# Kernel tuning notes

Measured on AMD Instinct MI355X. Metric: run time of the kernel, lower is better.

The kernel has to match this reference:

```python
import jax, jax.numpy as jnp
import numpy as np

EPS = 1e-12  # torch F.normalize eps
K = 32       # num_clusters (hardcoded in module)

def l2norm(v, axis):
    n = jnp.sqrt(jnp.sum(v * v, axis=axis, keepdims=True))
    return v / jnp.maximum(n, EPS)

def setup_inputs() -> dict:
    key = jax.random.key(0)
    k1, k2, k3, k4 = jax.random.split(key, 4)
    B, M, D = 64, 128, 2048
    x = jax.random.normal(k1, (B, M, D), dtype=jnp.float32)
    # ragged lengths in [1, M]
    lengths = jax.random.randint(k2, (B,), 0, M, dtype=jnp.int32) + 1
    init_sc = 1.0 / np.sqrt(D)
    W = init_sc * jax.random.normal(k3, (K, D), dtype=jnp.float32)  # fc1.weight
    C = init_sc * jax.random.normal(k4, (K, D), dtype=jnp.float32)  # centroids
    return {"x": x, "lengths": lengths, "W": W, "C": C}

def reference(x, lengths, W, C):
    # x: [B,M,D] padded frames, lengths: [B] valid frame counts
    B, M, D = x.shape
    mask = (jnp.arange(M)[None, :] < lengths[:, None]).astype(x.dtype)  # [B,M]
    cnt = lengths.astype(x.dtype)[:, None]                              # [B,1]
    # avg pooling over valid (raw, un-normalized) frames
    avgpool = jnp.sum(x * mask[:, :, None], axis=1) / cnt               # [B,D]
    # per-frame L2 normalize
    xn = l2norm(x, axis=-1)                                             # [B,M,D]
    # soft assignment: linear (no bias) + softmax over clusters
    logits = jnp.einsum('bmd,kd->bmk', xn, W)
    a = jax.nn.softmax(logits, axis=-1) * mask[:, :, None]              # [B,M,K]
    # VLAD residual aggregation, GEMM form:
    # sum_m a[b,m,k]*(xn[b,m,:] - C[k,:]) = (a^T xn) - C * sum_m a
    ax = jnp.einsum('bmk,bmd->bkd', a, xn)                              # [B,K,D]
    asum = jnp.sum(a, axis=1)                                           # [B,K]
    vlad = ax - asum[:, :, None] * C[None, :, :]                        # [B,K,D]
    # intra-normalize per cluster, flatten, global L2 normalize
    vlad = l2norm(vlad, axis=2)
    vlad = vlad.reshape(B, K * D)
    vlad = l2norm(vlad, axis=1)
    return jnp.concatenate([avgpool, vlad], axis=1)                     # [B, D + K*D]
```

## Files before the change

kernel.cpp:

```cpp
#include <hip/hip_runtime.h>
#include <math.h>

#define BB 64
#define MM 128
#define DDIM 2048
#define KK 32
#define NFR (BB*MM)
#define OUTROW (DDIM + KK*DDIM)

typedef __attribute__((ext_vector_type(8))) short bf16x8;
typedef __attribute__((ext_vector_type(4))) float f32x4;

__device__ __forceinline__ short f2bf(float f) {
  unsigned u = __builtin_bit_cast(unsigned, f);
  u += 0x7fffu + ((u >> 16) & 1u);
  return (short)(u >> 16);
}
__device__ __forceinline__ unsigned pack2(float lo, float hi) {
  return (unsigned)(unsigned short)f2bf(lo) | ((unsigned)(unsigned short)f2bf(hi) << 16);
}

__global__ __launch_bounds__(256) void k_prep(const float* __restrict__ W,
                                              short* __restrict__ Wb) {
  int i = (blockIdx.x * 256 + threadIdx.x) * 8;
  float4 a = *(const float4*)(W + i);
  float4 b = *(const float4*)(W + i + 4);
  bf16x8 o = {f2bf(a.x), f2bf(a.y), f2bf(a.z), f2bf(a.w),
              f2bf(b.x), f2bf(b.y), f2bf(b.z), f2bf(b.w)};
  *(bf16x8*)(Wb + i) = o;
}

__global__ __launch_bounds__(256, 2) void k_logits(const float* __restrict__ x,
    const int* __restrict__ lengths, const short* __restrict__ Wb,
    short* __restrict__ aT, float* __restrict__ asum_p) {
  const int t = threadIdx.x, wv = t >> 6, lane = t & 63;
  const int l15 = lane & 15, quad = lane >> 4;
  const int fg = blockIdx.x;
  const int g0 = fg * 16;
  const int b  = fg >> 3;
  const int m0 = (fg & 7) * 16;
  const int len = lengths[b];
  const bool av = (m0 + l15) < len;

  const float* xrow = x + (size_t)(g0 + l15) * DDIM + wv * 512 + quad * 8;
  const short* w0   = Wb + l15 * DDIM + wv * 512 + quad * 8;
  const short* w1   = w0 + 16 * DDIM;

  f32x4 c0 = {0.f, 0.f, 0.f, 0.f}, c1 = {0.f, 0.f, 0.f, 0.f};
  float ssq = 0.f;
  #pragma unroll
  for (int h = 0; h < 2; ++h) {
    float4 xa[8], xc[8];
    bf16x8 B0[8], B1[8];
    #pragma unroll
    for (int s = 0; s < 8; ++s) {
      const int so = h * 8 + s;
      if (av) {
        xa[s] = *(const float4*)(xrow + so * 32);
        xc[s] = *(const float4*)(xrow + so * 32 + 4);
      } else {
        xa[s] = make_float4(0.f, 0.f, 0.f, 0.f);
        xc[s] = make_float4(0.f, 0.f, 0.f, 0.f);
      }
      B0[s] = *(const bf16x8*)(w0 + so * 32);
      B1[s] = *(const bf16x8*)(w1 + so * 32);
    }
    #pragma unroll
    for (int s = 0; s < 8; ++s) {
      ssq = fmaf(xa[s].x, xa[s].x, ssq); ssq = fmaf(xa[s].y, xa[s].y, ssq);
      ssq = fmaf(xa[s].z, xa[s].z, ssq); ssq = fmaf(xa[s].w, xa[s].w, ssq);
      ssq = fmaf(xc[s].x, xc[s].x, ssq); ssq = fmaf(xc[s].y, xc[s].y, ssq);
      ssq = fmaf(xc[s].z, xc[s].z, ssq); ssq = fmaf(xc[s].w, xc[s].w, ssq);
      bf16x8 A = {f2bf(xa[s].x), f2bf(xa[s].y), f2bf(xa[s].z), f2bf(xa[s].w),
                  f2bf(xc[s].x), f2bf(xc[s].y), f2bf(xc[s].z), f2bf(xc[s].w)};
      c0 = __builtin_amdgcn_mfma_f32_16x16x32_bf16(A, B0[s], c0, 0, 0, 0);
      c1 = __builtin_amdgcn_mfma_f32_16x16x32_bf16(A, B1[s], c1, 0, 0, 0);
    }
  }

  ssq += __shfl_xor(ssq, 16, 64);
  ssq += __shfl_xor(ssq, 32, 64);
  __shared__ float sq[4][16];
  __shared__ float lg[4][16][33];
  if (quad == 0) sq[wv][l15] = ssq;
  #pragma unroll
  for (int r = 0; r < 4; ++r) {
    lg[wv][quad * 4 + r][l15]      = c0[r];
    lg[wv][quad * 4 + r][16 + l15] = c1[r];
  }
  __syncthreads();

  const int fr = t >> 4, kk = (t & 15) * 2;
  float s0 = 0.f, s1 = 0.f;
  #pragma unroll
  for (int w = 0; w < 4; ++w) { s0 += lg[w][fr][kk]; s1 += lg[w][fr][kk + 1]; }
  float ss  = sq[0][fr] + sq[1][fr] + sq[2][fr] + sq[3][fr];
  float inv = 1.f / fmaxf(sqrtf(ss), 1e-12f);
  s0 *= inv; s1 *= inv;
  float mx = fmaxf(s0, s1);
  mx = fmaxf(mx, __shfl_xor(mx, 1, 64));
  mx = fmaxf(mx, __shfl_xor(mx, 2, 64));
  mx = fmaxf(mx, __shfl_xor(mx, 4, 64));
  mx = fmaxf(mx, __shfl_xor(mx, 8, 64));
  float e0 = __expf(s0 - mx), e1 = __expf(s1 - mx);
  float se = e0 + e1;
  se += __shfl_xor(se, 1, 64);
  se += __shfl_xor(se, 2, 64);
  se += __shfl_xor(se, 4, 64);
  se += __shfl_xor(se, 8, 64);
  const bool valid = (m0 + fr) < len;
  float rr = valid ? (1.f / se) : 0.f;
  float a0 = e0 * rr, a1 = e1 * rr;

  __syncthreads();
  lg[0][fr][kk] = a0; lg[0][fr][kk + 1] = a1;
  __syncthreads();
  if (t < KK) {
    float s = 0.f;
    #pragma unroll
    for (int f = 0; f < 16; ++f) s += lg[0][f][t];
    asum_p[(size_t)fg * KK + t] = s;
  }
  short* ap = aT + (size_t)b * KK * MM + m0 + fr;
  ap[(size_t)kk * MM]       = f2bf(a0 * inv);
  ap[(size_t)(kk + 1) * MM] = f2bf(a1 * inv);
}

__global__ __launch_bounds__(256, 2) void k_vlad(const float* __restrict__ x,
    const int* __restrict__ lengths, const float* __restrict__ Cc,
    const short* __restrict__ aT, const float* __restrict__ asum_p,
    float* __restrict__ out, float* __restrict__ ssq_part) {
  const int t = threadIdx.x, wv = t >> 6, lane = t & 63;
  const int l15 = lane & 15, quad = lane >> 4;
  const int dc = blockIdx.x, b = blockIdx.y;
  const int dw0 = dc * 256 + wv * 64;
  const int len = lengths[b];

  __shared__ short xbt[4][64][40];
  __shared__ float asl[KK];
  __shared__ float ssw[4][33];

  if (t < KK) {
    float s = 0.f;
    #pragma unroll
    for (int p = 0; p < 8; ++p) s += asum_p[(size_t)(b * 8 + p) * KK + t];
    asl[t] = s;
  }

  const float* xb  = x  + (size_t)b * MM * DDIM;
  const short* at0 = aT + (size_t)b * KK * MM + l15 * MM + quad * 8;

  const int q4   = l15 * 4;
  const int mrow = quad * 2;
  const int keyw = l15 & 3;
  const int keyr = (l15 >> 2) & 3;

  bf16x8 A0[4], A1[4];
  #pragma unroll
  for (int ms = 0; ms < 4; ++ms) {
    A0[ms] = *(const bf16x8*)(at0 + ms * 32);
    A1[ms] = *(const bf16x8*)(at0 + 16 * MM + ms * 32);
  }

  float4 v0[16], v1[16];
  #pragma unroll
  for (int ms = 0; ms < 4; ++ms) {
    #pragma unroll
    for (int p = 0; p < 4; ++p) {
      const int m = ms * 32 + p * 8 + mrow;
      const float* xr = xb + (size_t)m * DDIM + dw0 + q4;
      v0[ms * 4 + p] = (m < len) ? *(const float4*)xr
                                 : make_float4(0.f, 0.f, 0.f, 0.f);
      v1[ms * 4 + p] = (m + 1 < len) ? *(const float4*)(xr + DDIM)
                                     : make_float4(0.f, 0.f, 0.f, 0.f);
    }
  }

  float avg[4] = {0.f, 0.f, 0.f, 0.f};
  #pragma unroll
  for (int i = 0; i < 16; ++i) {
    avg[0] += v0[i].x + v1[i].x;
    avg[1] += v0[i].y + v1[i].y;
    avg[2] += v0[i].z + v1[i].z;
    avg[3] += v0[i].w + v1[i].w;
  }

  f32x4 acc[2][4];
  #pragma unroll
  for (int kt = 0; kt < 2; ++kt)
    #pragma unroll
    for (int nt = 0; nt < 4; ++nt) acc[kt][nt] = (f32x4){0.f, 0.f, 0.f, 0.f};

  #pragma unroll
  for (int ms = 0; ms < 4; ++ms) {
    #pragma unroll
    for (int p = 0; p < 4; ++p) {
      const int i = ms * 4 + p;
      const int mls = (p ^ keyw) * 8 + mrow;
      *(unsigned*)&xbt[wv][q4 + 0][mls] = pack2(v0[i].x, v1[i].x);
      *(unsigned*)&xbt[wv][q4 + 1][mls] = pack2(v0[i].y, v1[i].y);
      *(unsigned*)&xbt[wv][q4 + 2][mls] = pack2(v0[i].z, v1[i].z);
      *(unsigned*)&xbt[wv][q4 + 3][mls] = pack2(v0[i].w, v1[i].w);
    }
    #pragma unroll
    for (int nt = 0; nt < 4; ++nt) {
      bf16x8 B = *(const bf16x8*)&xbt[wv][nt * 16 + l15][(quad ^ keyr) * 8];
      acc[0][nt] = __builtin_amdgcn_mfma_f32_16x16x32_bf16(A0[ms], B, acc[0][nt], 0, 0, 0);
      acc[1][nt] = __builtin_amdgcn_mfma_f32_16x16x32_bf16(A1[ms], B, acc[1][nt], 0, 0, 0);
    }
  }

  #pragma unroll
  for (int c = 0; c < 4; ++c) {
    avg[c] += __shfl_xor(avg[c], 16, 64);
    avg[c] += __shfl_xor(avg[c], 32, 64);
  }
  if (quad == 0) {
    float rl = 1.f / (float)len;
    *(float4*)(out + (size_t)b * OUTROW + dw0 + q4) =
        make_float4(avg[0] * rl, avg[1] * rl, avg[2] * rl, avg[3] * rl);
  }

  __syncthreads();
  float* orow = out + (size_t)b * OUTROW + DDIM;
  #pragma unroll
  for (int kt = 0; kt < 2; ++kt) {
    #pragma unroll
    for (int r = 0; r < 4; ++r) {
      const int k = kt * 16 + quad * 4 + r;
      const float as = asl[k];
      float sqv = 0.f;
      #pragma unroll
      for (int nt = 0; nt < 4; ++nt) {
        const int d = dw0 + nt * 16 + l15;
        float v = acc[kt][nt][r] - as * Cc[(size_t)k * DDIM + d];
        orow[(size_t)k * DDIM + d] = v;
        sqv = fmaf(v, v, sqv);
      }
      sqv += __shfl_xor(sqv, 1, 64);
      sqv += __shfl_xor(sqv, 2, 64);
      sqv += __shfl_xor(sqv, 4, 64);
      sqv += __shfl_xor(sqv, 8, 64);
      if (l15 == 0) ssw[wv][k] = sqv;
    }
  }
  __syncthreads();
  if (t < KK)
    ssq_part[((size_t)dc * BB + b) * KK + t] =
        ssw[0][t] + ssw[1][t] + ssw[2][t] + ssw[3][t];
}

__global__ __launch_bounds__(256) void k_norm(const float* __restrict__ ssq_part,
    float* __restrict__ out) {
  const int t = threadIdx.x;
  const int k = blockIdx.x;
  const int b = blockIdx.y;
  __shared__ float ssk[32];
  if (t < 32) {
    float sk = 0.f;
    #pragma unroll
    for (int dc = 0; dc < 8; ++dc)
      sk += ssq_part[((size_t)dc * BB + b) * KK + t];
    ssk[t] = sk;
  }
  __syncthreads();
  float gss = 0.f, iv_own = 0.f;
  #pragma unroll
  for (int kk = 0; kk < 32; ++kk) {
    float nk = sqrtf(ssk[kk]);
    float iv = 1.f / fmaxf(nk, 1e-12f);
    float nn = nk * iv;
    gss += nn * nn;
    if (kk == k) iv_own = iv;
  }
  float sc = iv_own / fmaxf(sqrtf(gss), 1e-12f);
  float* row = out + (size_t)b * OUTROW + DDIM + (size_t)k * DDIM;
  #pragma unroll
  for (int h = 0; h < 2; ++h) {
    float4* p = (float4*)(row + h * 1024 + t * 4);
    float4 v = *p;
    v.x *= sc; v.y *= sc; v.z *= sc; v.w *= sc;
    *p = v;
  }
}

extern "C" void kernel_launch(void* const* d_in, const int* in_sizes, int n_in,
                              void* d_out, int out_size, void* d_ws, size_t ws_size,
                              hipStream_t stream) {
  const float* x       = (const float*)d_in[0];
  const int*   lengths = (const int*)d_in[1];
  const float* W       = (const float*)d_in[2];
  const float* C       = (const float*)d_in[3];
  float* out = (float*)d_out;

  short* Wb     = (short*)d_ws;
  short* aT     = Wb + (size_t)KK * DDIM;
  float* asum_p = (float*)(aT + (size_t)BB * KK * MM);
  float* ssqp   = asum_p + (size_t)512 * KK;

  k_prep  <<<dim3(32),     256, 0, stream>>>(W, Wb);
  k_logits<<<dim3(512),    256, 0, stream>>>(x, lengths, Wb, aT, asum_p);
  k_vlad  <<<dim3(8, BB),  256, 0, stream>>>(x, lengths, C, aT, asum_p, out, ssqp);
  k_norm  <<<dim3(KK, BB), 256, 0, stream>>>(ssqp, out);
}
```

Before: 145.5 us.

## Fuse logits, VLAD, and normalization into one kernel with per-batch spin barriers

Measured after the change: 402.9 us. 2.77x slower.

```diff
diff --git a/kernel.cpp b/kernel.cpp
--- a/kernel.cpp
+++ b/kernel.cpp
@@ -5,7 +5,6 @@
 #define MM 128
 #define DDIM 2048
 #define KK 32
-#define NFR (BB*MM)
 #define OUTROW (DDIM + KK*DDIM)
 
 typedef __attribute__((ext_vector_type(8))) short bf16x8;
@@ -18,6 +17,21 @@
 }
 __device__ __forceinline__ unsigned pack2(float lo, float hi) {
   return (unsigned)(unsigned short)f2bf(lo) | ((unsigned)(unsigned short)f2bf(hi) << 16);
+}
+
+__device__ __forceinline__ void batch_barrier(int* bar) {
+  __syncthreads();
+  __threadfence();
+  if (threadIdx.x == 0) {
+    __hip_atomic_fetch_add(bar, 1, __ATOMIC_ACQ_REL, __HIP_MEMORY_SCOPE_AGENT);
+    int it = 0;
+    while (__hip_atomic_load(bar, __ATOMIC_ACQUIRE, __HIP_MEMORY_SCOPE_AGENT) < 8) {
+      __builtin_amdgcn_s_sleep(8);
+      if (++it > (1 << 20)) break;
+    }
+  }
+  __syncthreads();
+  __threadfence();
 }
 
 __global__ __launch_bounds__(256) void k_prep(const float* __restrict__ W,
@@ -30,257 +44,260 @@
   *(bf16x8*)(Wb + i) = o;
 }
 
-__global__ __launch_bounds__(256, 2) void k_logits(const float* __restrict__ x,
-    const int* __restrict__ lengths, const short* __restrict__ Wb,
-    short* __restrict__ aT, float* __restrict__ asum_p) {
+__global__ __launch_bounds__(256, 2) void k_main(
+    const float* __restrict__ x, const int* __restrict__ lengths,
+    const short* __restrict__ Wb, const float* __restrict__ Cc,
+    float* __restrict__ out, short* __restrict__ aT,
+    float* __restrict__ asum_p, float* __restrict__ ssq_part,
+    int* bar1, int* bar2) {
   const int t = threadIdx.x, wv = t >> 6, lane = t & 63;
   const int l15 = lane & 15, quad = lane >> 4;
-  const int fg = blockIdx.x;
-  const int g0 = fg * 16;
-  const int b  = fg >> 3;
-  const int m0 = (fg & 7) * 16;
+  const int bid = blockIdx.x;
+  const int b = bid >> 3, part = bid & 7;
+  const int m0 = part * 16;
   const int len = lengths[b];
-  const bool av = (m0 + l15) < len;
-
-  const float* xrow = x + (size_t)(g0 + l15) * DDIM + wv * 512 + quad * 8;
-  const short* w0   = Wb + l15 * DDIM + wv * 512 + quad * 8;
-  const short* w1   = w0 + 16 * DDIM;
-
-  f32x4 c0 = {0.f, 0.f, 0.f, 0.f}, c1 = {0.f, 0.f, 0.f, 0.f};
-  float ssq = 0.f;
-  #pragma unroll
-  for (int h = 0; h < 2; ++h) {
-    float4 xa[8], xc[8];
-    bf16x8 B0[8], B1[8];
-    #pragma unroll
-    for (int s = 0; s < 8; ++s) {
-      const int so = h * 8 + s;
-      if (av) {
-        xa[s] = *(const float4*)(xrow + so * 32);
-        xc[s] = *(const float4*)(xrow + so * 32 + 4);
-      } else {
-        xa[s] = make_float4(0.f, 0.f, 0.f, 0.f);
-        xc[s] = make_float4(0.f, 0.f, 0.f, 0.f);
-      }
-      B0[s] = *(const bf16x8*)(w0 + so * 32);
-      B1[s] = *(const bf16x8*)(w1 + so * 32);
-    }
-    #pragma unroll
-    for (int s = 0; s < 8; ++s) {
-      ssq = fmaf(xa[s].x, xa[s].x, ssq); ssq = fmaf(xa[s].y, xa[s].y, ssq);
-      ssq = fmaf(xa[s].z, xa[s].z, ssq); ssq = fmaf(xa[s].w, xa[s].w, ssq);
-      ssq = fmaf(xc[s].x, xc[s].x, ssq); ssq = fmaf(xc[s].y, xc[s].y, ssq);
-      ssq = fmaf(xc[s].z, xc[s].z, ssq); ssq = fmaf(xc[s].w, xc[s].w, ssq);
-      bf16x8 A = {f2bf(xa[s].x), f2bf(xa[s].y), f2bf(xa[s].z), f2bf(xa[s].w),
-                  f2bf(xc[s].x), f2bf(xc[s].y), f2bf(xc[s].z), f2bf(xc[s].w)};
-      c0 = __builtin_amdgcn_mfma_f32_16x16x32_bf16(A, B0[s], c0, 0, 0, 0);
-      c1 = __builtin_amdgcn_mfma_f32_16x16x32_bf16(A, B1[s], c1, 0, 0, 0);
-    }
-  }
-
-  ssq += __shfl_xor(ssq, 16, 64);
-  ssq += __shfl_xor(ssq, 32, 64);
+
   __shared__ float sq[4][16];
   __shared__ float lg[4][16][33];
-  if (quad == 0) sq[wv][l15] = ssq;
-  #pragma unroll
-  for (int r = 0; r < 4; ++r) {
-    lg[wv][quad * 4 + r][l15]      = c0[r];
-    lg[wv][quad * 4 + r][16 + l15] = c1[r];
-  }
-  __syncthreads();
-
-  const int fr = t >> 4, kk = (t & 15) * 2;
-  float s0 = 0.f, s1 = 0.f;
-  #pragma unroll
-  for (int w = 0; w < 4; ++w) { s0 += lg[w][fr][kk]; s1 += lg[w][fr][kk + 1]; }
-  float ss  = sq[0][fr] + sq[1][fr] + sq[2][fr] + sq[3][fr];
-  float inv = 1.f / fmaxf(sqrtf(ss), 1e-12f);
-  s0 *= inv; s1 *= inv;
-  float mx = fmaxf(s0, s1);
-  mx = fmaxf(mx, __shfl_xor(mx, 1, 64));
-  mx = fmaxf(mx, __shfl_xor(mx, 2, 64));
-  mx = fmaxf(mx, __shfl_xor(mx, 4, 64));
-  mx = fmaxf(mx, __shfl_xor(mx, 8, 64));
-  float e0 = __expf(s0 - mx), e1 = __expf(s1 - mx);
-  float se = e0 + e1;
-  se += __shfl_xor(se, 1, 64);
-  se += __shfl_xor(se, 2, 64);
-  se += __shfl_xor(se, 4, 64);
-  se += __shfl_xor(se, 8, 64);
-  const bool valid = (m0 + fr) < len;
-  float rr = valid ? (1.f / se) : 0.f;
-  float a0 = e0 * rr, a1 = e1 * rr;
-
-  __syncthreads();
-  lg[0][fr][kk] = a0; lg[0][fr][kk + 1] = a1;
-  __syncthreads();
-  if (t < KK) {
-    float s = 0.f;
-    #pragma unroll
-    for (int f = 0; f < 16; ++f) s += lg[0][f][t];
-    asum_p[(size_t)fg * KK + t] = s;
-  }
-  short* ap = aT + (size_t)b * KK * MM + m0 + fr;
-  ap[(size_t)kk * MM]       = f2bf(a0 * inv);
-  ap[(size_t)(kk + 1) * MM] = f2bf(a1 * inv);
-}
-
-__global__ __launch_bounds__(256, 2) void k_vlad(const float* __restrict__ x,
-    const int* __restrict__ lengths, const float* __restrict__ Cc,
-    const short* __restrict__ aT, const float* __restrict__ asum_p,
-    float* __restrict__ out, float* __restrict__ ssq_part) {
-  const int t = threadIdx.x, wv = t >> 6, lane = t & 63;
-  const int l15 = lane & 15, quad = lane >> 4;
-  const int dc = blockIdx.x, b = blockIdx.y;
-  const int dw0 = dc * 256 + wv * 64;
-  const int len = lengths[b];
-
   __shared__ short xbt[4][64][40];
   __shared__ float asl[KK];
   __shared__ float ssw[4][33];
-
-  if (t < KK) {
-    float s = 0.f;
-    #pragma unroll
-    for (int p = 0; p < 8; ++p) s += asum_p[(size_t)(b * 8 + p) * KK + t];
-    asl[t] = s;
+  __shared__ float ssk[KK];
+
+  if (m0 < len) {
+    const int g0 = bid * 16;
+    const bool av = (m0 + l15) < len;
+    const float* xrow = x + (size_t)(g0 + l15) * DDIM + wv * 512 + quad * 8;
+    const short* w0   = Wb + l15 * DDIM + wv * 512 + quad * 8;
+    const short* w1   = w0 + 16 * DDIM;
+
+    f32x4 c0 = {0.f, 0.f, 0.f, 0.f}, c1 = {0.f, 0.f, 0.f, 0.f};
+    float ssq = 0.f;
+    #pragma unroll
+    for (int h = 0; h < 2; ++h) {
+      float4 xa[8], xc[8];
+      bf16x8 B0[8], B1[8];
+      #pragma unroll
+      for (int s = 0; s < 8; ++s) {
+        const int so = h * 8 + s;
+        if (av) {
+          xa[s] = *(const float4*)(xrow + so * 32);
+          xc[s] = *(const float4*)(xrow + so * 32 + 4);
+        } else {
+          xa[s] = make_float4(0.f, 0.f, 0.f, 0.f);
+          xc[s] = make_float4(0.f, 0.f, 0.f, 0.f);
+        }
+        B0[s] = *(const bf16x8*)(w0 + so * 32);
+        B1[s] = *(const bf16x8*)(w1 + so * 32);
+      }
+      #pragma unroll
+      for (int s = 0; s < 8; ++s) {
+        ssq = fmaf(xa[s].x, xa[s].x, ssq); ssq = fmaf(xa[s].y, xa[s].y, ssq);
+        ssq = fmaf(xa[s].z, xa[s].z, ssq); ssq = fmaf(xa[s].w, xa[s].w, ssq);
+        ssq = fmaf(xc[s].x, xc[s].x, ssq); ssq = fmaf(xc[s].y, xc[s].y, ssq);
+        ssq = fmaf(xc[s].z, xc[s].z, ssq); ssq = fmaf(xc[s].w, xc[s].w, ssq);
+        bf16x8 A = {f2bf(xa[s].x), f2bf(xa[s].y), f2bf(xa[s].z), f2bf(xa[s].w),
+                    f2bf(xc[s].x), f2bf(xc[s].y), f2bf(xc[s].z), f2bf(xc[s].w)};
+        c0 = __builtin_amdgcn_mfma_f32_16x16x32_bf16(A, B0[s], c0, 0, 0, 0);
+        c1 = __builtin_amdgcn_mfma_f32_16x16x32_bf16(A, B1[s], c1, 0, 0, 0);
+      }
+    }
+
+    ssq += __shfl_xor(ssq, 16, 64);
+    ssq += __shfl_xor(ssq, 32, 64);
+    if (quad == 0) sq[wv][l15] = ssq;
+    #pragma unroll
+    for (int r = 0; r < 4; ++r) {
+      lg[wv][quad * 4 + r][l15]      = c0[r];
+      lg[wv][quad * 4 + r][16 + l15] = c1[r];
+    }
+    __syncthreads();
+
+    const int fr = t >> 4, kk = (t & 15) * 2;
+    float s0 = 0.f, s1 = 0.f;
+    #pragma unroll
+    for (int w = 0; w < 4; ++w) { s0 += lg[w][fr][kk]; s1 += lg[w][fr][kk + 1]; }
+    float ss  = sq[0][fr] + sq[1][fr] + sq[2][fr] + sq[3][fr];
+    float inv = 1.f / fmaxf(sqrtf(ss), 1e-12f);
+    s0 *= inv; s1 *= inv;
+    float mx = fmaxf(s0, s1);
+    mx = fmaxf(mx, __shfl_xor(mx, 1, 64));
+    mx = fmaxf(mx, __shfl_xor(mx, 2, 64));
+    mx = fmaxf(mx, __shfl_xor(mx, 4, 64));
+    mx = fmaxf(mx, __shfl_xor(mx, 8, 64));
+    float e0 = __expf(s0 - mx), e1 = __expf(s1 - mx);
+    float se = e0 + e1;
+    se += __shfl_xor(se, 1, 64);
+    se += __shfl_xor(se, 2, 64);
+    se += __shfl_xor(se, 4, 64);
+    se += __shfl_xor(se, 8, 64);
+    const bool valid = (m0 + fr) < len;
+    float rr = valid ? (1.f / se) : 0.f;
+    float a0 = e0 * rr, a1 = e1 * rr;
+
+    __syncthreads();
+    lg[0][fr][kk] = a0; lg[0][fr][kk + 1] = a1;
+    __syncthreads();
+    if (t < KK) {
+      float s = 0.f;
+      #pragma unroll
+      for (int f = 0; f < 16; ++f) s += lg[0][f][t];
+      asum_p[(size_t)bid * KK + t] = s;
+    }
+    short* ap = aT + (size_t)b * KK * MM + m0 + fr;
+    ap[(size_t)kk * MM]       = f2bf(a0 * inv);
+    ap[(size_t)(kk + 1) * MM] = f2bf(a1 * inv);
+  } else {
+    if (t < KK) asum_p[(size_t)bid * KK + t] = 0.f;
+    const int zk = t >> 3, zoff = (t & 7) * 2;
+    *(unsigned*)(aT + (size_t)b * KK * MM + (size_t)zk * MM + m0 + zoff) = 0u;
   }
-
-  const float* xb  = x  + (size_t)b * MM * DDIM;
-  const short* at0 = aT + (size_t)b * KK * MM + l15 * MM + quad * 8;
-
-  const int q4   = l15 * 4;
-  const int mrow = quad * 2;
-  const int keyw = l15 & 3;
-  const int keyr = (l15 >> 2) & 3;
-
-  bf16x8 A0[4], A1[4];
-  #pragma unroll
-  for (int ms = 0; ms < 4; ++ms) {
-    A0[ms] = *(const bf16x8*)(at0 + ms * 32);
-    A1[ms] = *(const bf16x8*)(at0 + 16 * MM + ms * 32);
+  batch_barrier(bar1 + b);
+
+  const int dc = part;
+  const int dw0 = dc * 256 + wv * 64;
+  f32x4 acc[2][4];
+  {
+    if (t < KK) {
+      float s = 0.f;
+      #pragma unroll
+      for (int p = 0; p < 8; ++p) s += asum_p[(size_t)(b * 8 + p) * KK + t];
+      asl[t] = s;
+    }
+
+    const float* xb  = x  + (size_t)b * MM * DDIM;
+    const short* at0 = aT + (size_t)b * KK * MM + l15 * MM + quad * 8;
+
+    const int q4   = l15 * 4;
+    const int mrow = quad * 2;
+    const int keyw = l15 & 3;
+    const int keyr = (l15 >> 2) & 3;
+
+    bf16x8 A0[4], A1[4];
+    #pragma unroll
+    for (int ms = 0; ms < 4; ++ms) {
+      A0[ms] = *(const bf16x8*)(at0 + ms * 32);
+      A1[ms] = *(const bf16x8*)(at0 + 16 * MM + ms * 32);
+    }
+
+    float4 v0[16], v1[16];
+    #pragma unroll
+    for (int ms = 0; ms < 4; ++ms) {
+      #pragma unroll
+      for (int p = 0; p < 4; ++p) {
+        const int m = ms * 32 + p * 8 + mrow;
+        const float* xr = xb + (size_t)m * DDIM + dw0 + q4;
+        v0[ms * 4 + p] = (m < len) ? *(const float4*)xr
+                                   : make_float4(0.f, 0.f, 0.f, 0.f);
+        v1[ms * 4 + p] = (m + 1 < len) ? *(const float4*)(xr + DDIM)
+                                       : make_float4(0.f, 0.f, 0.f, 0.f);
+      }
+    }
+
+    float avg[4] = {0.f, 0.f, 0.f, 0.f};
+    #pragma unroll
+    for (int i = 0; i < 16; ++i) {
+      avg[0] += v0[i].x + v1[i].x;
+      avg[1] += v0[i].y + v1[i].y;
+      avg[2] += v0[i].z + v1[i].z;
+      avg[3] += v0[i].w + v1[i].w;
+    }
+
+    #pragma unroll
+    for (int kt = 0; kt < 2; ++kt)
+      #pragma unroll
+      for (int nt = 0; nt < 4; ++nt) acc[kt][nt] = (f32x4){0.f, 0.f, 0.f, 0.f};
+
+    #pragma unroll
+    for (int ms = 0; ms < 4; ++ms) {
+      #pragma unroll
+      for (int p = 0; p < 4; ++p) {
+        const int i = ms * 4 + p;
+        const int mls = (p ^ keyw) * 8 + mrow;
+        *(unsigned*)&xbt[wv][q4 + 0][mls] = pack2(v0[i].x, v1[i].x);
+        *(unsigned*)&xbt[wv][q4 + 1][mls] = pack2(v0[i].y, v1[i].y);
+        *(unsigned*)&xbt[wv][q4 + 2][mls] = pack2(v0[i].z, v1[i].z);
+        *(unsigned*)&xbt[wv][q4 + 3][mls] = pack2(v0[i].w, v1[i].w);
+      }
+      #pragma unroll
+      for (int nt = 0; nt < 4; ++nt) {
+        bf16x8 B = *(const bf16x8*)&xbt[wv][nt * 16 + l15][(quad ^ keyr) * 8];
+        acc[0][nt] = __builtin_amdgcn_mfma_f32_16x16x32_bf16(A0[ms], B, acc[0][nt], 0, 0, 0);
+        acc[1][nt] = __builtin_amdgcn_mfma_f32_16x16x32_bf16(A1[ms], B, acc[1][nt], 0, 0, 0);
+      }
+    }
+
+    #pragma unroll
+    for (int c = 0; c < 4; ++c) {
+      avg[c] += __shfl_xor(avg[c], 16, 64);
+      avg[c] += __shfl_xor(avg[c], 32, 64);
+    }
+    if (quad == 0) {
+      float rl = 1.f / (float)len;
+      *(float4*)(out + (size_t)b * OUTROW + dw0 + q4) =
+          make_float4(avg[0] * rl, avg[1] * rl, avg[2] * rl, avg[3] * rl);
+    }
+
+    __syncthreads();
+    #pragma unroll
+    for (int kt = 0; kt < 2; ++kt) {
+      #pragma unroll
+      for (int r = 0; r < 4; ++r) {
+        const int k = kt * 16 + quad * 4 + r;
+        const float as = asl[k];
+        float sqv = 0.f;
+        #pragma unroll
+        for (int nt = 0; nt < 4; ++nt) {
+          const int d = dw0 + nt * 16 + l15;
+          float v = acc[kt][nt][r] - as * Cc[(size_t)k * DDIM + d];
+          acc[kt][nt][r] = v;
+          sqv = fmaf(v, v, sqv);
+        }
+        sqv += __shfl_xor(sqv, 1, 64);
+        sqv += __shfl_xor(sqv, 2, 64);
+        sqv += __shfl_xor(sqv, 4, 64);
+        sqv += __shfl_xor(sqv, 8, 64);
+        if (l15 == 0) ssw[wv][k] = sqv;
+      }
+    }
+    __syncthreads();
+    if (t < KK)
+      ssq_part[((size_t)dc * BB + b) * KK + t] =
+          ssw[0][t] + ssw[1][t] + ssw[2][t] + ssw[3][t];
   }
-
-  float4 v0[16], v1[16];
-  #pragma unroll
-  for (int ms = 0; ms < 4; ++ms) {
-    #pragma unroll
-    for (int p = 0; p < 4; ++p) {
-      const int m = ms * 32 + p * 8 + mrow;
-      const float* xr = xb + (size_t)m * DDIM + dw0 + q4;
-      v0[ms * 4 + p] = (m < len) ? *(const float4*)xr
-                                 : make_float4(0.f, 0.f, 0.f, 0.f);
-      v1[ms * 4 + p] = (m + 1 < len) ? *(const float4*)(xr + DDIM)
-                                     : make_float4(0.f, 0.f, 0.f, 0.f);
-    }
-  }
-
-  float avg[4] = {0.f, 0.f, 0.f, 0.f};
-  #pragma unroll
-  for (int i = 0; i < 16; ++i) {
-    avg[0] += v0[i].x + v1[i].x;
-    avg[1] += v0[i].y + v1[i].y;
-    avg[2] += v0[i].z + v1[i].z;
-    avg[3] += v0[i].w + v1[i].w;
-  }
-
-  f32x4 acc[2][4];
-  #pragma unroll
-  for (int kt = 0; kt < 2; ++kt)
-    #pragma unroll
-    for (int nt = 0; nt < 4; ++nt) acc[kt][nt] = (f32x4){0.f, 0.f, 0.f, 0.f};
-
-  #pragma unroll
-  for (int ms = 0; ms < 4; ++ms) {
-    #pragma unroll
-    for (int p = 0; p < 4; ++p) {
-      const int i = ms * 4 + p;
-      const int mls = (p ^ keyw) * 8 + mrow;
-      *(unsigned*)&xbt[wv][q4 + 0][mls] = pack2(v0[i].x, v1[i].x);
-      *(unsigned*)&xbt[wv][q4 + 1][mls] = pack2(v0[i].y, v1[i].y);
-      *(unsigned*)&xbt[wv][q4 + 2][mls] = pack2(v0[i].z, v1[i].z);
-      *(unsigned*)&xbt[wv][q4 + 3][mls] = pack2(v0[i].w, v1[i].w);
-    }
-    #pragma unroll
-    for (int nt = 0; nt < 4; ++nt) {
-      bf16x8 B = *(const bf16x8*)&xbt[wv][nt * 16 + l15][(quad ^ keyr) * 8];
-      acc[0][nt] = __builtin_amdgcn_mfma_f32_16x16x32_bf16(A0[ms], B, acc[0][nt], 0, 0, 0);
-      acc[1][nt] = __builtin_amdgcn_mfma_f32_16x16x32_bf16(A1[ms], B, acc[1][nt], 0, 0, 0);
-    }
-  }
-
-  #pragma unroll
-  for (int c = 0; c < 4; ++c) {
-    avg[c] += __shfl_xor(avg[c], 16, 64);
-    avg[c] += __shfl_xor(avg[c], 32, 64);
-  }
-  if (quad == 0) {
-    float rl = 1.f / (float)len;
-    *(float4*)(out + (size_t)b * OUTROW + dw0 + q4) =
-        make_float4(avg[0] * rl, avg[1] * rl, avg[2] * rl, avg[3] * rl);
-  }
-
-  __syncthreads();
-  float* orow = out + (size_t)b * OUTROW + DDIM;
-  #pragma unroll
-  for (int kt = 0; kt < 2; ++kt) {
-    #pragma unroll
-    for (int r = 0; r < 4; ++r) {
-      const int k = kt * 16 + quad * 4 + r;
-      const float as = asl[k];
-      float sqv = 0.f;
-      #pragma unroll
-      for (int nt = 0; nt < 4; ++nt) {
-        const int d = dw0 + nt * 16 + l15;
-        float v = acc[kt][nt][r] - as * Cc[(size_t)k * DDIM + d];
-        orow[(size_t)k * DDIM + d] = v;
-        sqv = fmaf(v, v, sqv);
-      }
-      sqv += __shfl_xor(sqv, 1, 64);
-      sqv += __shfl_xor(sqv, 2, 64);
-      sqv += __shfl_xor(sqv, 4, 64);
-      sqv += __shfl_xor(sqv, 8, 64);
-      if (l15 == 0) ssw[wv][k] = sqv;
-    }
-  }
-  __syncthreads();
-  if (t < KK)
-    ssq_part[((size_t)dc * BB + b) * KK + t] =
-        ssw[0][t] + ssw[1][t] + ssw[2][t] + ssw[3][t];
-}
-
-__global__ __launch_bounds__(256) void k_norm(const float* __restrict__ ssq_part,
-    float* __restrict__ out) {
-  const int t = threadIdx.x;
-  const int k = blockIdx.x;
-  const int b = blockIdx.y;
-  __shared__ float ssk[32];
-  if (t < 32) {
-    float sk = 0.f;
-    #pragma unroll
-    for (int dc = 0; dc < 8; ++dc)
-      sk += ssq_part[((size_t)dc * BB + b) * KK + t];
-    ssk[t] = sk;
-  }
-  __syncthreads();
-  float gss = 0.f, iv_own = 0.f;
-  #pragma unroll
-  for (int kk = 0; kk < 32; ++kk) {
-    float nk = sqrtf(ssk[kk]);
-    float iv = 1.f / fmaxf(nk, 1e-12f);
-    float nn = nk * iv;
-    gss += nn * nn;
-    if (kk == k) iv_own = iv;
-  }
-  float sc = iv_own / fmaxf(sqrtf(gss), 1e-12f);
-  float* row = out + (size_t)b * OUTROW + DDIM + (size_t)k * DDIM;
-  #pragma unroll
-  for (int h = 0; h < 2; ++h) {
-    float4* p = (float4*)(row + h * 1024 + t * 4);
-    float4 v = *p;
-    v.x *= sc; v.y *= sc; v.z *= sc; v.w *= sc;
-    *p = v;
+  batch_barrier(bar2 + b);
+
+  {
+    if (t < KK) {
+      float s = 0.f;
+      #pragma unroll
+      for (int d8 = 0; d8 < 8; ++d8)
+        s += ssq_part[((size_t)d8 * BB + b) * KK + t];
+      ssk[t] = s;
+    }
+    __syncthreads();
+    float gss = 0.f;
+    #pragma unroll
+    for (int kk2 = 0; kk2 < KK; ++kk2) {
+      float nk = sqrtf(ssk[kk2]);
+      float iv = 1.f / fmaxf(nk, 1e-12f);
+      float nn = nk * iv;
+      gss += nn * nn;
+    }
+    const float rg = 1.f / fmaxf(sqrtf(gss), 1e-12f);
+    float* orow = out + (size_t)b * OUTROW + DDIM;
+    #pragma unroll
+    for (int kt = 0; kt < 2; ++kt) {
+      #pragma unroll
+      for (int r = 0; r < 4; ++r) {
+        const int k = kt * 16 + quad * 4 + r;
+        const float iv = 1.f / fmaxf(sqrtf(ssk[k]), 1e-12f);
+        const float sc = iv * rg;
+        #pragma unroll
+        for (int nt = 0; nt < 4; ++nt)
+          orow[(size_t)k * DDIM + dw0 + nt * 16 + l15] = acc[kt][nt][r] * sc;
+      }
+    }
   }
 }
 
@@ -297,9 +314,10 @@
   short* aT     = Wb + (size_t)KK * DDIM;
   float* asum_p = (float*)(aT + (size_t)BB * KK * MM);
   float* ssqp   = asum_p + (size_t)512 * KK;
-
-  k_prep  <<<dim3(32),     256, 0, stream>>>(W, Wb);
-  k_logits<<<dim3(512),    256, 0, stream>>>(x, lengths, Wb, aT, asum_p);
-  k_vlad  <<<dim3(8, BB),  256, 0, stream>>>(x, lengths, C, aT, asum_p, out, ssqp);
-  k_norm  <<<dim3(KK, BB), 256, 0, stream>>>(ssqp, out);
-}
+  int*   bars   = (int*)(ssqp + (size_t)8 * BB * KK);
+
+  hipMemsetAsync(bars, 0, 2 * BB * sizeof(int), stream);
+  k_prep<<<dim3(32),  256, 0, stream>>>(W, Wb);
+  k_main<<<dim3(512), 256, 0, stream>>>(x, lengths, Wb, C, out, aT,
+                                        asum_p, ssqp, bars, bars + BB);
+}
```

## Fuse final normalization into VLAD kernel via last-block atomic; skip padded frame tiles

Applied to the files above, without the earlier changes.

New measurement: 183.8 us. 26.4% more time.

```diff
diff --git a/kernel.cpp b/kernel.cpp
--- a/kernel.cpp
+++ b/kernel.cpp
@@ -5,7 +5,6 @@
 #define MM 128
 #define DDIM 2048
 #define KK 32
-#define NFR (BB*MM)
 #define OUTROW (DDIM + KK*DDIM)
 
 typedef __attribute__((ext_vector_type(8))) short bf16x8;
@@ -40,8 +39,15 @@
   const int b  = fg >> 3;
   const int m0 = (fg & 7) * 16;
   const int len = lengths[b];
+
+  if (m0 >= len) {
+    if (t < KK) asum_p[(size_t)fg * KK + t] = 0.f;
+    const int zk = t >> 3, zoff = (t & 7) * 2;
+    *(unsigned*)(aT + (size_t)b * KK * MM + (size_t)zk * MM + m0 + zoff) = 0u;
+    return;
+  }
+
   const bool av = (m0 + l15) < len;
-
   const float* xrow = x + (size_t)(g0 + l15) * DDIM + wv * 512 + quad * 8;
   const short* w0   = Wb + l15 * DDIM + wv * 512 + quad * 8;
   const short* w1   = w0 + 16 * DDIM;
@@ -129,7 +135,7 @@
 __global__ __launch_bounds__(256, 2) void k_vlad(const float* __restrict__ x,
     const int* __restrict__ lengths, const float* __restrict__ Cc,
     const short* __restrict__ aT, const float* __restrict__ asum_p,
-    float* __restrict__ out, float* __restrict__ ssq_part) {
+    float* __restrict__ out, float* __restrict__ ssq_part, int* cnt) {
   const int t = threadIdx.x, wv = t >> 6, lane = t & 63;
   const int l15 = lane & 15, quad = lane >> 4;
   const int dc = blockIdx.x, b = blockIdx.y;
@@ -139,6 +145,9 @@
   __shared__ short xbt[4][64][40];
   __shared__ float asl[KK];
   __shared__ float ssw[4][33];
+  __shared__ float ssk[KK];
+  __shared__ float scl[KK];
+  __shared__ int lastf;
 
   if (t < KK) {
     float s = 0.f;
@@ -248,39 +257,45 @@
   if (t < KK)
     ssq_part[((size_t)dc * BB + b) * KK + t] =
         ssw[0][t] + ssw[1][t] + ssw[2][t] + ssw[3][t];
-}
-
-__global__ __launch_bounds__(256) void k_norm(const float* __restrict__ ssq_part,
-    float* __restrict__ out) {
-  const int t = threadIdx.x;
-  const int k = blockIdx.x;
-  const int b = blockIdx.y;
-  __shared__ float ssk[32];
-  if (t < 32) {
-    float sk = 0.f;
-    #pragma unroll
-    for (int dc = 0; dc < 8; ++dc)
-      sk += ssq_part[((size_t)dc * BB + b) * KK + t];
-    ssk[t] = sk;
-  }
-  __syncthreads();
-  float gss = 0.f, iv_own = 0.f;
-  #pragma unroll
-  for (int kk = 0; kk < 32; ++kk) {
-    float nk = sqrtf(ssk[kk]);
+
+  __syncthreads();
+  if (t == 0) {
+    __threadfence();
+    int old = __hip_atomic_fetch_add(cnt + b, 1, __ATOMIC_ACQ_REL,
+                                     __HIP_MEMORY_SCOPE_AGENT);
+    lastf = (old == 7);
+    if (old == 7) __threadfence();
+  }
+  __syncthreads();
+  if (!lastf) return;
+
+  if (t < KK) {
+    float s = 0.f;
+    #pragma unroll
+    for (int d8 = 0; d8 < 8; ++d8)
+      s += ssq_part[((size_t)d8 * BB + b) * KK + t];
+    ssk[t] = s;
+  }
+  __syncthreads();
+  float gss = 0.f;
+  #pragma unroll
+  for (int kk2 = 0; kk2 < KK; ++kk2) {
+    float nk = sqrtf(ssk[kk2]);
     float iv = 1.f / fmaxf(nk, 1e-12f);
     float nn = nk * iv;
     gss += nn * nn;
-    if (kk == k) iv_own = iv;
-  }
-  float sc = iv_own / fmaxf(sqrtf(gss), 1e-12f);
-  float* row = out + (size_t)b * OUTROW + DDIM + (size_t)k * DDIM;
-  #pragma unroll
-  for (int h = 0; h < 2; ++h) {
-    float4* p = (float4*)(row + h * 1024 + t * 4);
-    float4 v = *p;
-    v.x *= sc; v.y *= sc; v.z *= sc; v.w *= sc;
-    *p = v;
+  }
+  const float rg = 1.f / fmaxf(sqrtf(gss), 1e-12f);
+  if (t < KK) scl[t] = rg / fmaxf(sqrtf(ssk[t]), 1e-12f);
+  __syncthreads();
+  #pragma unroll
+  for (int kk2 = 0; kk2 < KK; ++kk2) {
+    const float sc = scl[kk2];
+    float4* row = (float4*)(orow + (size_t)kk2 * DDIM);
+    float4 u0 = row[t], u1 = row[t + 256];
+    u0.x *= sc; u0.y *= sc; u0.z *= sc; u0.w *= sc;
+    u1.x *= sc; u1.y *= sc; u1.z *= sc; u1.w *= sc;
+    row[t] = u0; row[t + 256] = u1;
   }
 }
 
@@ -297,9 +312,11 @@
   short* aT     = Wb + (size_t)KK * DDIM;
   float* asum_p = (float*)(aT + (size_t)BB * KK * MM);
   float* ssqp   = asum_p + (size_t)512 * KK;
-
-  k_prep  <<<dim3(32),     256, 0, stream>>>(W, Wb);
-  k_logits<<<dim3(512),    256, 0, stream>>>(x, lengths, Wb, aT, asum_p);
-  k_vlad  <<<dim3(8, BB),  256, 0, stream>>>(x, lengths, C, aT, asum_p, out, ssqp);
-  k_norm  <<<dim3(KK, BB), 256, 0, stream>>>(ssqp, out);
-}
+  int*   cnt    = (int*)(ssqp + (size_t)8 * BB * KK);
+
+  hipMemsetAsync(cnt, 0, BB * sizeof(int), stream);
+  k_prep  <<<dim3(32),    256, 0, stream>>>(W, Wb);
+  k_logits<<<dim3(512),   256, 0, stream>>>(x, lengths, Wb, aT, asum_p);
+  k_vlad  <<<dim3(8, BB), 256, 0, stream>>>(x, lengths, C, aT, asum_p,
+                                            out, ssqp, cnt);
+}
```

## Split VLAD kernel over frame halves with LDS reduction; skip empty frame groups

Applied to the files above, without the earlier changes.

Result: no change. 143.1 us (-1.7%).

```diff
diff --git a/kernel.cpp b/kernel.cpp
--- a/kernel.cpp
+++ b/kernel.cpp
@@ -5,7 +5,7 @@
 #define MM 128
 #define DDIM 2048
 #define KK 32
-#define NFR (BB*MM)
+#define NDC 16
 #define OUTROW (DDIM + KK*DDIM)
 
 typedef __attribute__((ext_vector_type(8))) short bf16x8;
@@ -40,8 +40,15 @@
   const int b  = fg >> 3;
   const int m0 = (fg & 7) * 16;
   const int len = lengths[b];
+
+  if (m0 >= len) {
+    if (t < KK) asum_p[(size_t)fg * KK + t] = 0.f;
+    const int zk = t >> 3, zoff = (t & 7) * 2;
+    *(unsigned*)(aT + (size_t)b * KK * MM + (size_t)zk * MM + m0 + zoff) = 0u;
+    return;
+  }
+
   const bool av = (m0 + l15) < len;
-
   const float* xrow = x + (size_t)(g0 + l15) * DDIM + wv * 512 + quad * 8;
   const short* w0   = Wb + l15 * DDIM + wv * 512 + quad * 8;
   const short* w1   = w0 + 16 * DDIM;
@@ -126,19 +133,24 @@
   ap[(size_t)(kk + 1) * MM] = f2bf(a1 * inv);
 }
 
-__global__ __launch_bounds__(256, 2) void k_vlad(const float* __restrict__ x,
+__global__ __launch_bounds__(256, 4) void k_vlad(const float* __restrict__ x,
     const int* __restrict__ lengths, const float* __restrict__ Cc,
     const short* __restrict__ aT, const float* __restrict__ asum_p,
     float* __restrict__ out, float* __restrict__ ssq_part) {
   const int t = threadIdx.x, wv = t >> 6, lane = t & 63;
   const int l15 = lane & 15, quad = lane >> 4;
   const int dc = blockIdx.x, b = blockIdx.y;
-  const int dw0 = dc * 256 + wv * 64;
+  const int dh = wv & 1, mh = wv >> 1;
+  const int dwb = dc * 128 + dh * 64;
+  const int mb  = mh * 64;
   const int len = lengths[b];
 
-  __shared__ short xbt[4][64][40];
-  __shared__ float asl[KK];
-  __shared__ float ssw[4][33];
+  __shared__ __attribute__((aligned(16))) char ubuf[20480];
+  short (*xbt)[64][40]     = (short(*)[64][40])ubuf;
+  float (*exch)[2][64][20] = (float(*)[2][64][20])ubuf;
+  __shared__ float  asl[KK];
+  __shared__ float4 avp[2][16];
+  __shared__ float  ssw[4][17];
 
   if (t < KK) {
     float s = 0.f;
@@ -148,27 +160,27 @@
   }
 
   const float* xb  = x  + (size_t)b * MM * DDIM;
-  const short* at0 = aT + (size_t)b * KK * MM + l15 * MM + quad * 8;
+  const short* at0 = aT + (size_t)b * KK * MM + l15 * MM + mb + quad * 8;
 
   const int q4   = l15 * 4;
   const int mrow = quad * 2;
   const int keyw = l15 & 3;
   const int keyr = (l15 >> 2) & 3;
 
-  bf16x8 A0[4], A1[4];
-  #pragma unroll
-  for (int ms = 0; ms < 4; ++ms) {
+  bf16x8 A0[2], A1[2];
+  #pragma unroll
+  for (int ms = 0; ms < 2; ++ms) {
     A0[ms] = *(const bf16x8*)(at0 + ms * 32);
     A1[ms] = *(const bf16x8*)(at0 + 16 * MM + ms * 32);
   }
 
-  float4 v0[16], v1[16];
-  #pragma unroll
-  for (int ms = 0; ms < 4; ++ms) {
+  float4 v0[8], v1[8];
+  #pragma unroll
+  for (int ms = 0; ms < 2; ++ms) {
     #pragma unroll
     for (int p = 0; p < 4; ++p) {
-      const int m = ms * 32 + p * 8 + mrow;
-      const float* xr = xb + (size_t)m * DDIM + dw0 + q4;
+      const int m = mb + ms * 32 + p * 8 + mrow;
+      const float* xr = xb + (size_t)m * DDIM + dwb + q4;
       v0[ms * 4 + p] = (m < len) ? *(const float4*)xr
                                  : make_float4(0.f, 0.f, 0.f, 0.f);
       v1[ms * 4 + p] = (m + 1 < len) ? *(const float4*)(xr + DDIM)
@@ -178,21 +190,29 @@
 
   float avg[4] = {0.f, 0.f, 0.f, 0.f};
   #pragma unroll
-  for (int i = 0; i < 16; ++i) {
+  for (int i = 0; i < 8; ++i) {
     avg[0] += v0[i].x + v1[i].x;
     avg[1] += v0[i].y + v1[i].y;
     avg[2] += v0[i].z + v1[i].z;
     avg[3] += v0[i].w + v1[i].w;
   }
-
-  f32x4 acc[2][4];
-  #pragma unroll
-  for (int kt = 0; kt < 2; ++kt)
-    #pragma unroll
-    for (int nt = 0; nt < 4; ++nt) acc[kt][nt] = (f32x4){0.f, 0.f, 0.f, 0.f};
-
-  #pragma unroll
-  for (int ms = 0; ms < 4; ++ms) {
+  #pragma unroll
+  for (int c = 0; c < 4; ++c) {
+    avg[c] += __shfl_xor(avg[c], 16, 64);
+    avg[c] += __shfl_xor(avg[c], 32, 64);
+  }
+  if (mh == 1 && quad == 0)
+    avp[dh][l15] = make_float4(avg[0], avg[1], avg[2], avg[3]);
+
+  f32x4 acc0[4], acc1[4];
+  #pragma unroll
+  for (int nt = 0; nt < 4; ++nt) {
+    acc0[nt] = (f32x4){0.f, 0.f, 0.f, 0.f};
+    acc1[nt] = (f32x4){0.f, 0.f, 0.f, 0.f};
+  }
+
+  #pragma unroll
+  for (int ms = 0; ms < 2; ++ms) {
     #pragma unroll
     for (int p = 0; p < 4; ++p) {
       const int i = ms * 4 + p;
@@ -205,49 +225,62 @@
     #pragma unroll
     for (int nt = 0; nt < 4; ++nt) {
       bf16x8 B = *(const bf16x8*)&xbt[wv][nt * 16 + l15][(quad ^ keyr) * 8];
-      acc[0][nt] = __builtin_amdgcn_mfma_f32_16x16x32_bf16(A0[ms], B, acc[0][nt], 0, 0, 0);
-      acc[1][nt] = __builtin_amdgcn_mfma_f32_16x16x32_bf16(A1[ms], B, acc[1][nt], 0, 0, 0);
-    }
-  }
-
-  #pragma unroll
-  for (int c = 0; c < 4; ++c) {
-    avg[c] += __shfl_xor(avg[c], 16, 64);
-    avg[c] += __shfl_xor(avg[c], 32, 64);
-  }
-  if (quad == 0) {
+      acc0[nt] = __builtin_amdgcn_mfma_f32_16x16x32_bf16(A0[ms], B, acc0[nt], 0, 0, 0);
+      acc1[nt] = __builtin_amdgcn_mfma_f32_16x16x32_bf16(A1[ms], B, acc1[nt], 0, 0, 0);
+    }
+  }
+
+  f32x4 keep[4], give[4];
+  if (mh == 0) {
+    #pragma unroll
+    for (int nt = 0; nt < 4; ++nt) { keep[nt] = acc0[nt]; give[nt] = acc1[nt]; }
+  } else {
+    #pragma unroll
+    for (int nt = 0; nt < 4; ++nt) { keep[nt] = acc1[nt]; give[nt] = acc0[nt]; }
+  }
+
+  __syncthreads();
+  #pragma unroll
+  for (int nt = 0; nt < 4; ++nt)
+    *(f32x4*)&exch[dh][mh][lane][nt * 4] = give[nt];
+
+  if (mh == 0 && quad == 0) {
+    float4 pa = avp[dh][l15];
     float rl = 1.f / (float)len;
-    *(float4*)(out + (size_t)b * OUTROW + dw0 + q4) =
-        make_float4(avg[0] * rl, avg[1] * rl, avg[2] * rl, avg[3] * rl);
-  }
-
-  __syncthreads();
+    *(float4*)(out + (size_t)b * OUTROW + dwb + q4) =
+        make_float4((avg[0] + pa.x) * rl, (avg[1] + pa.y) * rl,
+                    (avg[2] + pa.z) * rl, (avg[3] + pa.w) * rl);
+  }
+
+  __syncthreads();
+  #pragma unroll
+  for (int nt = 0; nt < 4; ++nt)
+    keep[nt] += *(const f32x4*)&exch[dh][1 - mh][lane][nt * 4];
+
   float* orow = out + (size_t)b * OUTROW + DDIM;
   #pragma unroll
-  for (int kt = 0; kt < 2; ++kt) {
-    #pragma unroll
-    for (int r = 0; r < 4; ++r) {
-      const int k = kt * 16 + quad * 4 + r;
-      const float as = asl[k];
-      float sqv = 0.f;
-      #pragma unroll
-      for (int nt = 0; nt < 4; ++nt) {
-        const int d = dw0 + nt * 16 + l15;
-        float v = acc[kt][nt][r] - as * Cc[(size_t)k * DDIM + d];
-        orow[(size_t)k * DDIM + d] = v;
-        sqv = fmaf(v, v, sqv);
-      }
-      sqv += __shfl_xor(sqv, 1, 64);
-      sqv += __shfl_xor(sqv, 2, 64);
-      sqv += __shfl_xor(sqv, 4, 64);
-      sqv += __shfl_xor(sqv, 8, 64);
-      if (l15 == 0) ssw[wv][k] = sqv;
-    }
-  }
-  __syncthreads();
-  if (t < KK)
-    ssq_part[((size_t)dc * BB + b) * KK + t] =
-        ssw[0][t] + ssw[1][t] + ssw[2][t] + ssw[3][t];
+  for (int r = 0; r < 4; ++r) {
+    const int k = mh * 16 + quad * 4 + r;
+    const float as = asl[k];
+    float sqv = 0.f;
+    #pragma unroll
+    for (int nt = 0; nt < 4; ++nt) {
+      const int d = dwb + nt * 16 + l15;
+      float v = keep[nt][r] - as * Cc[(size_t)k * DDIM + d];
+      orow[(size_t)k * DDIM + d] = v;
+      sqv = fmaf(v, v, sqv);
+    }
+    sqv += __shfl_xor(sqv, 1, 64);
+    sqv += __shfl_xor(sqv, 2, 64);
+    sqv += __shfl_xor(sqv, 4, 64);
+    sqv += __shfl_xor(sqv, 8, 64);
+    if (l15 == 0) ssw[wv][quad * 4 + r] = sqv;
+  }
+  __syncthreads();
+  if (t < KK) {
+    const int mt = t >> 4, kl = t & 15;
+    ssq_part[((size_t)dc * BB + b) * KK + t] = ssw[mt * 2][kl] + ssw[mt * 2 + 1][kl];
+  }
 }
 
 __global__ __launch_bounds__(256) void k_norm(const float* __restrict__ ssq_part,
@@ -259,7 +292,7 @@
   if (t < 32) {
     float sk = 0.f;
     #pragma unroll
-    for (int dc = 0; dc < 8; ++dc)
+    for (int dc = 0; dc < NDC; ++dc)
       sk += ssq_part[((size_t)dc * BB + b) * KK + t];
     ssk[t] = sk;
   }
@@ -298,8 +331,8 @@
   float* asum_p = (float*)(aT + (size_t)BB * KK * MM);
   float* ssqp   = asum_p + (size_t)512 * KK;
 
-  k_prep  <<<dim3(32),     256, 0, stream>>>(W, Wb);
-  k_logits<<<dim3(512),    256, 0, stream>>>(x, lengths, Wb, aT, asum_p);
-  k_vlad  <<<dim3(8, BB),  256, 0, stream>>>(x, lengths, C, aT, asum_p, out, ssqp);
-  k_norm  <<<dim3(KK, BB), 256, 0, stream>>>(ssqp, out);
-}
+  k_prep  <<<dim3(32),      256, 0, stream>>>(W, Wb);
+  k_logits<<<dim3(512),     256, 0, stream>>>(x, lengths, Wb, aT, asum_p);
+  k_vlad  <<<dim3(NDC, BB), 256, 0, stream>>>(x, lengths, C, aT, asum_p, out, ssqp);
+  k_norm  <<<dim3(KK, BB),  256, 0, stream>>>(ssqp, out);
+}
```
